# Performance work log

Hardware: AMD Instinct MI355X
Metric: run time of the kernel (lower is better)

## Reference

```python
import jax, jax.numpy as jnp
import numpy as np

VOCAB_SIZE = 32000
HIDDEN_DIM = 1024
NUM_BUF_ACTIONS = 128
BATCH = 64
SEQ_LEN = 512


def setup_inputs() -> dict:
    key = jax.random.key(0)
    ks = jax.random.split(key, 8)
    H = HIDDEN_DIM
    x = jax.random.randint(ks[0], (BATCH, SEQ_LEN), 0, VOCAB_SIZE, dtype=jnp.int32)
    true_actions = jax.random.randint(ks[1], (BATCH, SEQ_LEN), 0, NUM_BUF_ACTIONS, dtype=jnp.int32)
    true_states = jax.random.randint(ks[2], (BATCH, SEQ_LEN), 0, NUM_BUF_ACTIONS, dtype=jnp.int32)
    use_forcing = 0
    # Learned params: embedding table, LSTM input/recurrent kernels (gate order i,f,g,o), dense head
    embed = jax.random.normal(ks[3], (VOCAB_SIZE, H), dtype=jnp.float32) * 0.02
    Wi = jax.random.normal(ks[4], (H, 4 * H), dtype=jnp.float32) * (1.0 / np.sqrt(H))
    Wh = jax.random.normal(ks[5], (H, 4 * H), dtype=jnp.float32) * (1.0 / np.sqrt(H))
    bh = jnp.zeros((4 * H,), dtype=jnp.float32)
    Wo = jax.random.normal(ks[6], (H, NUM_BUF_ACTIONS), dtype=jnp.float32) * (1.0 / np.sqrt(H))
    bo = jnp.zeros((NUM_BUF_ACTIONS,), dtype=jnp.float32)
    return {"embed": embed, "Wi": Wi, "Wh": Wh, "bh": bh, "Wo": Wo, "bo": bo,
            "x": x, "true_actions": true_actions, "true_states": true_states,
            "use_forcing": use_forcing}


def _lstm_forward(embed, Wi, Wh, bh, Wo, bo, x):
    B, S = x.shape
    H = embed.shape[1]
    x_emb = embed[x]                                    # [B,S,H]
    # Precompute input-side gate projections for all timesteps (one big GEMM)
    gx = jnp.einsum('bsh,hg->sbg', x_emb, Wi)           # [S,B,4H]
    c0 = jnp.zeros((B, H), dtype=x_emb.dtype)
    h0 = jnp.zeros((B, H), dtype=x_emb.dtype)

    def step(carry, gx_t):
        c, h = carry
        gates = gx_t + h @ Wh + bh                      # [B,4H]
        i, f, g, o = jnp.split(gates, 4, axis=-1)
        i = jax.nn.sigmoid(i)
        f = jax.nn.sigmoid(f)
        g = jnp.tanh(g)
        o = jax.nn.sigmoid(o)
        c = f * c + i * g
        h = o * jnp.tanh(c)
        return (c, h), h

    _, hs = jax.lax.scan(step, (c0, h0), gx)            # hs: [S,B,H]
    hs = jnp.transpose(hs, (1, 0, 2))                   # [B,S,H]
    logits_buf = hs @ Wo + bo                           # [B,S,A]
    dummy = jnp.zeros((B, S, 1), dtype=logits_buf.dtype)
    return dummy, logits_buf, dummy


def reference(embed, Wi, Wh, bh, Wo, bo, x, true_actions, true_states, use_forcing):
    # true_actions/true_states/use_forcing are unused in the original forward
    return _lstm_forward(embed, Wi, Wh, bh, Wo, bo, x)
```

## Files before the change

kernel.cpp:

```cpp
#include <hip/hip_runtime.h>
#include <hip/hip_bf16.h>

typedef __attribute__((ext_vector_type(8))) short short8;
typedef __attribute__((ext_vector_type(4))) float float4v;
typedef __attribute__((ext_vector_type(4))) unsigned int uint4v;
typedef unsigned short ushort_t;
typedef unsigned int uint_t;

#define BB 64
#define SS 512
#define HH 1024
#define AA 128
#define NWG 256

#define XSW_BYTES   67108864ULL
#define WSW_BYTES   16777216ULL
#define HALL_BYTES  67239936ULL
#define XSW_OFF     0ULL
#define WSW_OFF     (XSW_OFF + XSW_BYTES)
#define HALL_OFF    (WSW_OFF + WSW_BYTES)
#define FLAGS_OFF   (HALL_OFF + HALL_BYTES)

__device__ __forceinline__ ushort_t f2bf(float f) {
    union { float f; uint_t u; } v; v.f = f;
    uint_t u = v.u;
    return (ushort_t)((u + 0x7fffu + ((u >> 16) & 1u)) >> 16);
}

__device__ __forceinline__ float fast_sigmoid(float x) {
    return __builtin_amdgcn_rcpf(1.0f + __expf(-x));
}
__device__ __forceinline__ float fast_tanh(float x) {
    return 1.0f - 2.0f * __builtin_amdgcn_rcpf(1.0f + __expf(2.0f * x));
}

__global__ void k_init(uint_t* __restrict__ flags, ushort_t* __restrict__ hall,
                       float* __restrict__ out) {
    int i = blockIdx.x * 256 + threadIdx.x;
    if (i < NWG) flags[i] = 0u;
    ((uint_t*)hall)[i] = 0u;
    out[i] = 0.0f;
    out[32768 + (size_t)BB * SS * AA + i] = 0.0f;
}

__global__ void k_prep_x(const float* __restrict__ embed, const int* __restrict__ x,
                         ushort_t* __restrict__ xsw) {
    int t = blockIdx.x * 256 + threadIdx.x;
    int lane = t & 63;
    int rg   = (t >> 6) & 3;
    int kk   = (t >> 8) & 31;
    int s    = t >> 13;
    int b  = rg * 16 + (lane & 15);
    int k0 = kk * 32 + (lane >> 4) * 8;
    int tok = x[b * SS + s];
    const float* src = embed + (size_t)tok * HH + k0;
    float4v v0 = *(const float4v*)src;
    float4v v1 = *(const float4v*)(src + 4);
    uint_t p0 = (uint_t)f2bf(v0[0]) | ((uint_t)f2bf(v0[1]) << 16);
    uint_t p1 = (uint_t)f2bf(v0[2]) | ((uint_t)f2bf(v0[3]) << 16);
    uint_t p2 = (uint_t)f2bf(v1[0]) | ((uint_t)f2bf(v1[1]) << 16);
    uint_t p3 = (uint_t)f2bf(v1[2]) | ((uint_t)f2bf(v1[3]) << 16);
    uint4v pk = {p0, p1, p2, p3};
    ((uint4v*)xsw)[t] = pk;
}

__global__ void k_prep_w(const float* __restrict__ Wi, const float* __restrict__ Wh,
                         ushort_t* __restrict__ wsw) {
    int t = blockIdx.x * 256 + threadIdx.x;
    int u = t & 1023;
    int q = (t >> 10) & 3;
    int k = t >> 12;
    float v = (k < 1024) ? Wi[(size_t)k * 4096 + q * 1024 + u]
                         : Wh[(size_t)(k - 1024) * 4096 + q * 1024 + u];
    int g = u >> 2, du = u & 3;
    int c = du * 4 + q;
    int kk = k >> 5, quad = (k >> 3) & 3, j = k & 7;
    int lane = quad * 16 + c;
    wsw[(((size_t)g * 64 + kk) * 64 + lane) * 8 + j] = f2bf(v);
}

__global__ void __launch_bounds__(256)
k_lstm(const ushort_t* __restrict__ xsw, const ushort_t* __restrict__ wsw,
       ushort_t* hall, const float* __restrict__ bh, uint_t* flags) {
    __shared__ ushort_t wlds[64 * 64 * 8];
    const int g    = blockIdx.x;
    const int tid  = threadIdx.x;
    const int lane = tid & 63;
    const int rg   = tid >> 6;

    {
        const uint4v* src = (const uint4v*)(wsw + (size_t)g * 64 * 64 * 8);
        uint4v* dst = (uint4v*)wlds;
        for (int i = tid; i < 4096; i += 256) dst[i] = src[i];
    }
    __syncthreads();

    const int c_idx = lane & 15;
    const int q  = c_idx & 3;
    const int du = c_idx >> 2;
    const int quad = lane >> 4;
    const int u = g * 4 + du;
    const float bhv = bh[q * 1024 + u];

    const int kk_h = u >> 5;
    const int quad_h = (u & 31) >> 3;
    const int j_h = u & 7;
    uint_t* hall32 = (uint_t*)hall;

    float cst0 = 0.f, cst1 = 0.f, cst2 = 0.f, cst3 = 0.f;
    const short8* xbase = (const short8*)xsw;
    const short8* hbase = (const short8*)hall;
    const short8* wl = (const short8*)wlds + lane;

    for (int s = 0; s < SS; ++s) {
        float4v ac0 = {bhv, bhv, bhv, bhv};
        float4v ac1 = {0.f, 0.f, 0.f, 0.f};
        float4v ac2 = {0.f, 0.f, 0.f, 0.f};
        float4v ac3 = {0.f, 0.f, 0.f, 0.f};

        const short8* xp = xbase + (((size_t)s * 32) * 4 + rg) * 64 + lane;
        #pragma unroll
        for (int kk = 0; kk < 32; kk += 4) {
            short8 a0 = xp[(kk + 0) * 256];
            short8 a1 = xp[(kk + 1) * 256];
            short8 a2 = xp[(kk + 2) * 256];
            short8 a3 = xp[(kk + 3) * 256];
            ac0 = __builtin_amdgcn_mfma_f32_16x16x32_bf16(a0, wl[(kk + 0) * 64], ac0, 0, 0, 0);
            ac1 = __builtin_amdgcn_mfma_f32_16x16x32_bf16(a1, wl[(kk + 1) * 64], ac1, 0, 0, 0);
            ac2 = __builtin_amdgcn_mfma_f32_16x16x32_bf16(a2, wl[(kk + 2) * 64], ac2, 0, 0, 0);
            ac3 = __builtin_amdgcn_mfma_f32_16x16x32_bf16(a3, wl[(kk + 3) * 64], ac3, 0, 0, 0);
        }

        {
            bool ok;
            do {
                uint_t f = __hip_atomic_load(&flags[tid], __ATOMIC_RELAXED,
                                             __HIP_MEMORY_SCOPE_AGENT);
                ok = (f >= (uint_t)s);
            } while (!__syncthreads_and(ok));
            asm volatile("" ::: "memory");
        }

        const short8* hp = hbase + (((size_t)s * 32) * 4 + rg) * 64 + lane;
        #pragma unroll
        for (int kk = 0; kk < 32; kk += 4) {
            short8 a0 = hp[(kk + 0) * 256];
            short8 a1 = hp[(kk + 1) * 256];
            short8 a2 = hp[(kk + 2) * 256];
            short8 a3 = hp[(kk + 3) * 256];
            ac0 = __builtin_amdgcn_mfma_f32_16x16x32_bf16(a0, wl[(32 + kk + 0) * 64], ac0, 0, 0, 0);
            ac1 = __builtin_amdgcn_mfma_f32_16x16x32_bf16(a1, wl[(32 + kk + 1) * 64], ac1, 0, 0, 0);
            ac2 = __builtin_amdgcn_mfma_f32_16x16x32_bf16(a2, wl[(32 + kk + 2) * 64], ac2, 0, 0, 0);
            ac3 = __builtin_amdgcn_mfma_f32_16x16x32_bf16(a3, wl[(32 + kk + 3) * 64], ac3, 0, 0, 0);
        }
        float4v acc = (ac0 + ac1) + (ac2 + ac3);

        float hv[4];
        #pragma unroll
        for (int r = 0; r < 4; ++r) {
            float own = acc[r];
            float a = (q == 2) ? fast_tanh(own) : fast_sigmoid(own);
            float x1 = __shfl_xor(a, 1);
            float x2 = __shfl_xor(a, 2);
            float x3 = __shfl_xor(a, 3);
            float gi, gf, gg, go;
            if      (q == 0) { gi = a;  gf = x1; gg = x2; go = x3; }
            else if (q == 1) { gi = x1; gf = a;  gg = x3; go = x2; }
            else if (q == 2) { gi = x2; gf = x3; gg = a;  go = x1; }
            else             { gi = x3; gf = x2; gg = x1; go = a;  }
            float cv = (r == 0 ? cst0 : r == 1 ? cst1 : r == 2 ? cst2 : cst3);
            cv = gf * cv + gi * gg;
            if (r == 0) cst0 = cv; else if (r == 1) cst1 = cv;
            else if (r == 2) cst2 = cv; else cst3 = cv;
            hv[r] = go * fast_tanh(cv);
        }

        float pv0 = __shfl_xor(hv[0], 4);
        float pv1 = __shfl_xor(hv[1], 4);
        float pv2 = __shfl_xor(hv[2], 4);
        float pv3 = __shfl_xor(hv[3], 4);
        if (q == 0 && (du & 1) == 0) {
            float pv[4] = {pv0, pv1, pv2, pv3};
            size_t base = (((size_t)(s + 1) * 32 + kk_h) * 4 + rg) * 64;
            #pragma unroll
            for (int r = 0; r < 4; ++r) {
                uint_t packed = (uint_t)f2bf(hv[r]) | ((uint_t)f2bf(pv[r]) << 16);
                int lane_h = quad_h * 16 + quad * 4 + r;
                size_t idx = ((base + (size_t)lane_h) * 8 + j_h) >> 1;
                __hip_atomic_store(&hall32[idx], packed, __ATOMIC_RELAXED,
                                   __HIP_MEMORY_SCOPE_AGENT);
            }
        }
        __syncthreads();
        if (tid == 0)
            __hip_atomic_store(&flags[g], (uint_t)(s + 1), __ATOMIC_RELAXED,
                               __HIP_MEMORY_SCOPE_AGENT);
    }
}

__global__ void __launch_bounds__(256)
k_head(const ushort_t* __restrict__ hall, const float* __restrict__ Wo,
       const float* __restrict__ bo, float* __restrict__ out) {
    __shared__ ushort_t wlds[32 * 2 * 64 * 8];
    const int wg = blockIdx.x;
    const int cg = wg & 3, sg = wg >> 2;
    const int tid = threadIdx.x, lane = tid & 63, rg = tid >> 6;
    const int col0 = cg * 32;

    for (int i = tid; i < 32768; i += 256) {
        int k = i >> 5;
        int col = i & 31;
        float v = Wo[(size_t)k * AA + col0 + col];
        int kk = k >> 5, quad = (k >> 3) & 3, j = k & 7;
        int nt = col >> 4, cl = col & 15;
        wlds[(((kk * 2 + nt) * 64) + quad * 16 + cl) * 8 + j] = f2bf(v);
    }
    __syncthreads();

    const int cl = lane & 15, quad = lane >> 4;
    const float bo0 = bo[col0 + cl];
    const float bo1 = bo[col0 + 16 + cl];
    const short8* wl = (const short8*)wlds + lane;

    for (int si = 0; si < 4; ++si) {
        int s = sg * 4 + si;
        float4v a0 = {bo0, bo0, bo0, bo0};
        float4v a1 = {bo1, bo1, bo1, bo1};
        const short8* hp = (const short8*)hall + (((size_t)(s + 1) * 32) * 4 + rg) * 64 + lane;
        #pragma unroll 8
        for (int kk = 0; kk < 32; ++kk) {
            short8 a = hp[kk * 256];
            a0 = __builtin_amdgcn_mfma_f32_16x16x32_bf16(a, wl[(kk * 2 + 0) * 64], a0, 0, 0, 0);
            a1 = __builtin_amdgcn_mfma_f32_16x16x32_bf16(a, wl[(kk * 2 + 1) * 64], a1, 0, 0, 0);
        }
        #pragma unroll
        for (int r = 0; r < 4; ++r) {
            int b = rg * 16 + quad * 4 + r;
            size_t o = 32768 + ((size_t)b * SS + s) * AA;
            out[o + col0 + cl]      = a0[r];
            out[o + col0 + 16 + cl] = a1[r];
        }
    }
}

extern "C" void kernel_launch(void* const* d_in, const int* in_sizes, int n_in,
                              void* d_out, int out_size, void* d_ws, size_t ws_size,
                              hipStream_t stream) {
    const float* embed = (const float*)d_in[0];
    const float* Wi    = (const float*)d_in[1];
    const float* Wh    = (const float*)d_in[2];
    const float* bh    = (const float*)d_in[3];
    const float* Wo    = (const float*)d_in[4];
    const float* bo    = (const float*)d_in[5];
    const int*   x     = (const int*)d_in[6];
    float* out = (float*)d_out;
    unsigned char* ws = (unsigned char*)d_ws;

    ushort_t* xsw  = (ushort_t*)(ws + XSW_OFF);
    ushort_t* wsw  = (ushort_t*)(ws + WSW_OFF);
    ushort_t* hall = (ushort_t*)(ws + HALL_OFF);
    uint_t*   flags = (uint_t*)(ws + FLAGS_OFF);

    k_init  <<<128,   256, 0, stream>>>(flags, hall, out);
    k_prep_x<<<16384, 256, 0, stream>>>(embed, x, xsw);
    k_prep_w<<<32768, 256, 0, stream>>>(Wi, Wh, wsw);
    k_lstm  <<<NWG,   256, 0, stream>>>(xsw, wsw, hall, bh, flags);
    k_head  <<<512,   256, 0, stream>>>(hall, Wo, bo, out);
}
```

Before: 2.795 ms.

## Split LSTM into producer WGs for input projections and consumer WGs for recurrence

```diff
diff --git a/kernel.cpp b/kernel.cpp
--- a/kernel.cpp
+++ b/kernel.cpp
@@ -6,12 +6,14 @@
 typedef __attribute__((ext_vector_type(4))) unsigned int uint4v;
 typedef unsigned short ushort_t;
 typedef unsigned int uint_t;
+typedef unsigned long long ull_t;
 
 #define BB 64
 #define SS 512
 #define HH 1024
 #define AA 128
-#define NWG 256
+#define NCG 128
+#define RSLOTS 8
 
 #define XSW_BYTES   67108864ULL
 #define WSW_BYTES   16777216ULL
@@ -20,13 +22,19 @@
 #define WSW_OFF     (XSW_OFF + XSW_BYTES)
 #define HALL_OFF    (WSW_OFF + WSW_BYTES)
 #define FLAGS_OFF   (HALL_OFF + HALL_BYTES)
+#define RING_OFF    (FLAGS_OFF + 4096ULL)
+#define RING_BYTES  (RSLOTS * 128ULL * 2ULL * 256ULL * 8ULL)
+
+#define MFMA __builtin_amdgcn_mfma_f32_16x16x32_bf16
 
 __device__ __forceinline__ ushort_t f2bf(float f) {
     union { float f; uint_t u; } v; v.f = f;
     uint_t u = v.u;
     return (ushort_t)((u + 0x7fffu + ((u >> 16) & 1u)) >> 16);
 }
-
+__device__ __forceinline__ float bf2f(ushort_t u) {
+    union { uint_t u; float f; } v; v.u = (uint_t)u << 16; return v.f;
+}
 __device__ __forceinline__ float fast_sigmoid(float x) {
     return __builtin_amdgcn_rcpf(1.0f + __expf(-x));
 }
@@ -37,7 +45,7 @@
 __global__ void k_init(uint_t* __restrict__ flags, ushort_t* __restrict__ hall,
                        float* __restrict__ out) {
     int i = blockIdx.x * 256 + threadIdx.x;
-    if (i < NWG) flags[i] = 0u;
+    if (i < 256) flags[i] = 0u;
     ((uint_t*)hall)[i] = 0u;
     out[i] = 0.0f;
     out[32768 + (size_t)BB * SS * AA + i] = 0.0f;
@@ -80,18 +88,21 @@
 }
 
 __global__ void __launch_bounds__(256)
-k_lstm(const ushort_t* __restrict__ xsw, const ushort_t* __restrict__ wsw,
-       ushort_t* hall, const float* __restrict__ bh, uint_t* flags) {
-    __shared__ ushort_t wlds[64 * 64 * 8];
-    const int g    = blockIdx.x;
+k_lstm2(const ushort_t* __restrict__ xsw, const ushort_t* __restrict__ wsw,
+        ushort_t* hall, const float* __restrict__ bh, uint_t* flags, ull_t* ring) {
+    __shared__ ushort_t wlds[2 * 32 * 64 * 8 + 11264];
     const int tid  = threadIdx.x;
     const int lane = tid & 63;
     const int rg   = tid >> 6;
+    const bool producer = (blockIdx.x >= NCG);
+    const int  wg = producer ? (blockIdx.x - NCG) : blockIdx.x;
 
     {
-        const uint4v* src = (const uint4v*)(wsw + (size_t)g * 64 * 64 * 8);
+        const int kkoff = producer ? 0 : 32;
+        const uint4v* s0 = (const uint4v*)(wsw + ((size_t)(2 * wg)     * 64 + kkoff) * 512);
+        const uint4v* s1 = (const uint4v*)(wsw + ((size_t)(2 * wg + 1) * 64 + kkoff) * 512);
         uint4v* dst = (uint4v*)wlds;
-        for (int i = tid; i < 4096; i += 256) dst[i] = src[i];
+        for (int i = tid; i < 2048; i += 256) { dst[i] = s0[i]; dst[2048 + i] = s1[i]; }
     }
     __syncthreads();
 
@@ -99,101 +110,149 @@
     const int q  = c_idx & 3;
     const int du = c_idx >> 2;
     const int quad = lane >> 4;
-    const int u = g * 4 + du;
-    const float bhv = bh[q * 1024 + u];
-
-    const int kk_h = u >> 5;
-    const int quad_h = (u & 31) >> 3;
-    const int j_h = u & 7;
+    const short8* wl = (const short8*)wlds + lane;
+
+    if (producer) {
+        const float bhv0 = bh[q * 1024 + (2 * wg)     * 4 + du];
+        const float bhv1 = bh[q * 1024 + (2 * wg + 1) * 4 + du];
+        const short8* xbase = (const short8*)xsw;
+        for (int s = 0; s < SS; ++s) {
+            float4v a00 = {bhv0, bhv0, bhv0, bhv0};
+            float4v a01 = {0.f, 0.f, 0.f, 0.f};
+            float4v a10 = {bhv1, bhv1, bhv1, bhv1};
+            float4v a11 = {0.f, 0.f, 0.f, 0.f};
+            const short8* xp = xbase + (((size_t)s * 32) * 4 + rg) * 64 + lane;
+            #pragma unroll
+            for (int kk = 0; kk < 32; kk += 2) {
+                short8 f0 = xp[(kk + 0) * 256];
+                short8 f1 = xp[(kk + 1) * 256];
+                a00 = MFMA(f0, wl[(kk + 0) * 64], a00, 0, 0, 0);
+                a10 = MFMA(f0, wl[(32 + kk + 0) * 64], a10, 0, 0, 0);
+                a01 = MFMA(f1, wl[(kk + 1) * 64], a01, 0, 0, 0);
+                a11 = MFMA(f1, wl[(32 + kk + 1) * 64], a11, 0, 0, 0);
+            }
+            float4v g0 = a00 + a01;
+            float4v g1 = a10 + a11;
+            {
+                int need = s - (RSLOTS - 1);
+                if (need > 0) {
+                    while ((int)__hip_atomic_load(&flags[wg], __ATOMIC_RELAXED,
+                                                  __HIP_MEMORY_SCOPE_AGENT) < need)
+                        __builtin_amdgcn_s_sleep(2);
+                }
+            }
+            ull_t* rp = ring + ((size_t)(s & (RSLOTS - 1)) * 128 + wg) * 512 + tid;
+            uint_t d0 = (uint_t)f2bf(g0[0]) | ((uint_t)f2bf(g0[1]) << 16);
+            uint_t d1 = (uint_t)f2bf(g0[2]) | ((uint_t)f2bf(g0[3]) << 16);
+            __hip_atomic_store(&rp[0], (ull_t)d0 | ((ull_t)d1 << 32),
+                               __ATOMIC_RELAXED, __HIP_MEMORY_SCOPE_AGENT);
+            uint_t e0 = (uint_t)f2bf(g1[0]) | ((uint_t)f2bf(g1[1]) << 16);
+            uint_t e1 = (uint_t)f2bf(g1[2]) | ((uint_t)f2bf(g1[3]) << 16);
+            __hip_atomic_store(&rp[256], (ull_t)e0 | ((ull_t)e1 << 32),
+                               __ATOMIC_RELAXED, __HIP_MEMORY_SCOPE_AGENT);
+            __syncthreads();
+            if (tid == 0)
+                __hip_atomic_store(&flags[128 + wg], (uint_t)(s + 1),
+                                   __ATOMIC_RELAXED, __HIP_MEMORY_SCOPE_AGENT);
+        }
+        return;
+    }
+
     uint_t* hall32 = (uint_t*)hall;
-
-    float cst0 = 0.f, cst1 = 0.f, cst2 = 0.f, cst3 = 0.f;
-    const short8* xbase = (const short8*)xsw;
     const short8* hbase = (const short8*)hall;
-    const short8* wl = (const short8*)wlds + lane;
+    float cst[2][4];
+    #pragma unroll
+    for (int t = 0; t < 2; ++t)
+        #pragma unroll
+        for (int r = 0; r < 4; ++r) cst[t][r] = 0.f;
 
     for (int s = 0; s < SS; ++s) {
-        float4v ac0 = {bhv, bhv, bhv, bhv};
-        float4v ac1 = {0.f, 0.f, 0.f, 0.f};
-        float4v ac2 = {0.f, 0.f, 0.f, 0.f};
-        float4v ac3 = {0.f, 0.f, 0.f, 0.f};
-
-        const short8* xp = xbase + (((size_t)s * 32) * 4 + rg) * 64 + lane;
-        #pragma unroll
-        for (int kk = 0; kk < 32; kk += 4) {
-            short8 a0 = xp[(kk + 0) * 256];
-            short8 a1 = xp[(kk + 1) * 256];
-            short8 a2 = xp[(kk + 2) * 256];
-            short8 a3 = xp[(kk + 3) * 256];
-            ac0 = __builtin_amdgcn_mfma_f32_16x16x32_bf16(a0, wl[(kk + 0) * 64], ac0, 0, 0, 0);
-            ac1 = __builtin_amdgcn_mfma_f32_16x16x32_bf16(a1, wl[(kk + 1) * 64], ac1, 0, 0, 0);
-            ac2 = __builtin_amdgcn_mfma_f32_16x16x32_bf16(a2, wl[(kk + 2) * 64], ac2, 0, 0, 0);
-            ac3 = __builtin_amdgcn_mfma_f32_16x16x32_bf16(a3, wl[(kk + 3) * 64], ac3, 0, 0, 0);
-        }
-
         {
+            const uint_t* addr = (tid < 128) ? &flags[tid] : &flags[128 + wg];
+            const uint_t need  = (tid < 128) ? (uint_t)s : (uint_t)(s + 1);
             bool ok;
             do {
-                uint_t f = __hip_atomic_load(&flags[tid], __ATOMIC_RELAXED,
+                uint_t f = __hip_atomic_load(addr, __ATOMIC_RELAXED,
                                              __HIP_MEMORY_SCOPE_AGENT);
-                ok = (f >= (uint_t)s);
+                ok = (f >= need);
             } while (!__syncthreads_and(ok));
             asm volatile("" ::: "memory");
         }
 
+        const ull_t* rp = ring + ((size_t)(s & (RSLOTS - 1)) * 128 + wg) * 512 + tid;
+        ull_t gx0 = __hip_atomic_load(&rp[0],   __ATOMIC_RELAXED, __HIP_MEMORY_SCOPE_AGENT);
+        ull_t gx1 = __hip_atomic_load(&rp[256], __ATOMIC_RELAXED, __HIP_MEMORY_SCOPE_AGENT);
+
+        float4v a00 = {0.f, 0.f, 0.f, 0.f};
+        float4v a01 = {0.f, 0.f, 0.f, 0.f};
+        float4v a10 = {0.f, 0.f, 0.f, 0.f};
+        float4v a11 = {0.f, 0.f, 0.f, 0.f};
         const short8* hp = hbase + (((size_t)s * 32) * 4 + rg) * 64 + lane;
         #pragma unroll
-        for (int kk = 0; kk < 32; kk += 4) {
-            short8 a0 = hp[(kk + 0) * 256];
-            short8 a1 = hp[(kk + 1) * 256];
-            short8 a2 = hp[(kk + 2) * 256];
-            short8 a3 = hp[(kk + 3) * 256];
-            ac0 = __builtin_amdgcn_mfma_f32_16x16x32_bf16(a0, wl[(32 + kk + 0) * 64], ac0, 0, 0, 0);
-            ac1 = __builtin_amdgcn_mfma_f32_16x16x32_bf16(a1, wl[(32 + kk + 1) * 64], ac1, 0, 0, 0);
-            ac2 = __builtin_amdgcn_mfma_f32_16x16x32_bf16(a2, wl[(32 + kk + 2) * 64], ac2, 0, 0, 0);
-            ac3 = __builtin_amdgcn_mfma_f32_16x16x32_bf16(a3, wl[(32 + kk + 3) * 64], ac3, 0, 0, 0);
-        }
-        float4v acc = (ac0 + ac1) + (ac2 + ac3);
-
-        float hv[4];
-        #pragma unroll
-        for (int r = 0; r < 4; ++r) {
-            float own = acc[r];
-            float a = (q == 2) ? fast_tanh(own) : fast_sigmoid(own);
-            float x1 = __shfl_xor(a, 1);
-            float x2 = __shfl_xor(a, 2);
-            float x3 = __shfl_xor(a, 3);
-            float gi, gf, gg, go;
-            if      (q == 0) { gi = a;  gf = x1; gg = x2; go = x3; }
-            else if (q == 1) { gi = x1; gf = a;  gg = x3; go = x2; }
-            else if (q == 2) { gi = x2; gf = x3; gg = a;  go = x1; }
-            else             { gi = x3; gf = x2; gg = x1; go = a;  }
-            float cv = (r == 0 ? cst0 : r == 1 ? cst1 : r == 2 ? cst2 : cst3);
-            cv = gf * cv + gi * gg;
-            if (r == 0) cst0 = cv; else if (r == 1) cst1 = cv;
-            else if (r == 2) cst2 = cv; else cst3 = cv;
-            hv[r] = go * fast_tanh(cv);
-        }
-
-        float pv0 = __shfl_xor(hv[0], 4);
-        float pv1 = __shfl_xor(hv[1], 4);
-        float pv2 = __shfl_xor(hv[2], 4);
-        float pv3 = __shfl_xor(hv[3], 4);
-        if (q == 0 && (du & 1) == 0) {
-            float pv[4] = {pv0, pv1, pv2, pv3};
-            size_t base = (((size_t)(s + 1) * 32 + kk_h) * 4 + rg) * 64;
+        for (int kk = 0; kk < 32; kk += 2) {
+            short8 f0 = hp[(kk + 0) * 256];
+            short8 f1 = hp[(kk + 1) * 256];
+            a00 = MFMA(f0, wl[(kk + 0) * 64], a00, 0, 0, 0);
+            a10 = MFMA(f0, wl[(32 + kk + 0) * 64], a10, 0, 0, 0);
+            a01 = MFMA(f1, wl[(kk + 1) * 64], a01, 0, 0, 0);
+            a11 = MFMA(f1, wl[(32 + kk + 1) * 64], a11, 0, 0, 0);
+        }
+        float4v acc0 = a00 + a01;
+        float4v acc1 = a10 + a11;
+        acc0[0] += bf2f((ushort_t)gx0);
+        acc0[1] += bf2f((ushort_t)(gx0 >> 16));
+        acc0[2] += bf2f((ushort_t)(gx0 >> 32));
+        acc0[3] += bf2f((ushort_t)(gx0 >> 48));
+        acc1[0] += bf2f((ushort_t)gx1);
+        acc1[1] += bf2f((ushort_t)(gx1 >> 16));
+        acc1[2] += bf2f((ushort_t)(gx1 >> 32));
+        acc1[3] += bf2f((ushort_t)(gx1 >> 48));
+
+        float hv[2][4];
+        #pragma unroll
+        for (int t = 0; t < 2; ++t) {
             #pragma unroll
             for (int r = 0; r < 4; ++r) {
-                uint_t packed = (uint_t)f2bf(hv[r]) | ((uint_t)f2bf(pv[r]) << 16);
-                int lane_h = quad_h * 16 + quad * 4 + r;
-                size_t idx = ((base + (size_t)lane_h) * 8 + j_h) >> 1;
-                __hip_atomic_store(&hall32[idx], packed, __ATOMIC_RELAXED,
-                                   __HIP_MEMORY_SCOPE_AGENT);
+                float own = t ? acc1[r] : acc0[r];
+                float a = (q == 2) ? fast_tanh(own) : fast_sigmoid(own);
+                float x1 = __shfl_xor(a, 1);
+                float x2 = __shfl_xor(a, 2);
+                float x3 = __shfl_xor(a, 3);
+                float gi, gf, gg, go;
+                if      (q == 0) { gi = a;  gf = x1; gg = x2; go = x3; }
+                else if (q == 1) { gi = x1; gf = a;  gg = x3; go = x2; }
+                else if (q == 2) { gi = x2; gf = x3; gg = a;  go = x1; }
+                else             { gi = x3; gf = x2; gg = x1; go = a;  }
+                float cv = gf * cst[t][r] + gi * gg;
+                cst[t][r] = cv;
+                hv[t][r] = go * fast_tanh(cv);
+            }
+        }
+
+        #pragma unroll
+        for (int t = 0; t < 2; ++t) {
+            float p0 = __shfl_xor(hv[t][0], 4);
+            float p1 = __shfl_xor(hv[t][1], 4);
+            float p2 = __shfl_xor(hv[t][2], 4);
+            float p3 = __shfl_xor(hv[t][3], 4);
+            if (q == 0 && (du & 1) == 0) {
+                int u = (2 * wg + t) * 4 + du;
+                int kk_h = u >> 5, quad_h = (u & 31) >> 3, j_h = u & 7;
+                size_t base = (((size_t)(s + 1) * 32 + kk_h) * 4 + rg) * 64;
+                float pv[4] = {p0, p1, p2, p3};
+                #pragma unroll
+                for (int r = 0; r < 4; ++r) {
+                    uint_t packed = (uint_t)f2bf(hv[t][r]) | ((uint_t)f2bf(pv[r]) << 16);
+                    int lane_h = quad_h * 16 + quad * 4 + r;
+                    size_t idx = ((base + (size_t)lane_h) * 8 + j_h) >> 1;
+                    __hip_atomic_store(&hall32[idx], packed, __ATOMIC_RELAXED,
+                                       __HIP_MEMORY_SCOPE_AGENT);
+                }
             }
         }
         __syncthreads();
         if (tid == 0)
-            __hip_atomic_store(&flags[g], (uint_t)(s + 1), __ATOMIC_RELAXED,
+            __hip_atomic_store(&flags[wg], (uint_t)(s + 1), __ATOMIC_RELAXED,
                                __HIP_MEMORY_SCOPE_AGENT);
     }
 }
@@ -230,8 +289,8 @@
         #pragma unroll 8
         for (int kk = 0; kk < 32; ++kk) {
             short8 a = hp[kk * 256];
-            a0 = __builtin_amdgcn_mfma_f32_16x16x32_bf16(a, wl[(kk * 2 + 0) * 64], a0, 0, 0, 0);
-            a1 = __builtin_amdgcn_mfma_f32_16x16x32_bf16(a, wl[(kk * 2 + 1) * 64], a1, 0, 0, 0);
+            a0 = MFMA(a, wl[(kk * 2 + 0) * 64], a0, 0, 0, 0);
+            a1 = MFMA(a, wl[(kk * 2 + 1) * 64], a1, 0, 0, 0);
         }
         #pragma unroll
         for (int r = 0; r < 4; ++r) {
@@ -256,14 +315,15 @@
     float* out = (float*)d_out;
     unsigned char* ws = (unsigned char*)d_ws;
 
-    ushort_t* xsw  = (ushort_t*)(ws + XSW_OFF);
-    ushort_t* wsw  = (ushort_t*)(ws + WSW_OFF);
-    ushort_t* hall = (ushort_t*)(ws + HALL_OFF);
+    ushort_t* xsw   = (ushort_t*)(ws + XSW_OFF);
+    ushort_t* wsw   = (ushort_t*)(ws + WSW_OFF);
+    ushort_t* hall  = (ushort_t*)(ws + HALL_OFF);
     uint_t*   flags = (uint_t*)(ws + FLAGS_OFF);
+    ull_t*    ring  = (ull_t*)(ws + RING_OFF);
 
     k_init  <<<128,   256, 0, stream>>>(flags, hall, out);
     k_prep_x<<<16384, 256, 0, stream>>>(embed, x, xsw);
     k_prep_w<<<32768, 256, 0, stream>>>(Wi, Wh, wsw);
-    k_lstm  <<<NWG,   256, 0, stream>>>(xsw, wsw, hall, bh, flags);
+    k_lstm2 <<<256,   256, 0, stream>>>(xsw, wsw, hall, bh, flags, ring);
     k_head  <<<512,   256, 0, stream>>>(hall, Wo, bo, out);
 }
```

New measurement: 5.186 ms. +85.6%, slower.

## Split barrier signal and wait around x-projection work in persistent LSTM

Applied to the files above, without the earlier changes.

```diff
diff --git a/kernel.cpp b/kernel.cpp
--- a/kernel.cpp
+++ b/kernel.cpp
@@ -20,6 +20,8 @@
 #define WSW_OFF     (XSW_OFF + XSW_BYTES)
 #define HALL_OFF    (WSW_OFF + WSW_BYTES)
 #define FLAGS_OFF   (HALL_OFF + HALL_BYTES)
+
+#define MFMA __builtin_amdgcn_mfma_f32_16x16x32_bf16
 
 __device__ __forceinline__ ushort_t f2bf(float f) {
     union { float f; uint_t u; } v; v.f = f;
@@ -82,7 +84,7 @@
 __global__ void __launch_bounds__(256)
 k_lstm(const ushort_t* __restrict__ xsw, const ushort_t* __restrict__ wsw,
        ushort_t* hall, const float* __restrict__ bh, uint_t* flags) {
-    __shared__ ushort_t wlds[64 * 64 * 8];
+    __shared__ ushort_t wlds[64 * 64 * 8 + 10240];
     const int g    = blockIdx.x;
     const int tid  = threadIdx.x;
     const int lane = tid & 63;
@@ -106,11 +108,11 @@
     const int quad_h = (u & 31) >> 3;
     const int j_h = u & 7;
     uint_t* hall32 = (uint_t*)hall;
-
-    float cst0 = 0.f, cst1 = 0.f, cst2 = 0.f, cst3 = 0.f;
     const short8* xbase = (const short8*)xsw;
     const short8* hbase = (const short8*)hall;
     const short8* wl = (const short8*)wlds + lane;
+
+    float cst0 = 0.f, cst1 = 0.f, cst2 = 0.f, cst3 = 0.f;
 
     for (int s = 0; s < SS; ++s) {
         float4v ac0 = {bhv, bhv, bhv, bhv};
@@ -119,25 +121,51 @@
         float4v ac3 = {0.f, 0.f, 0.f, 0.f};
 
         const short8* xp = xbase + (((size_t)s * 32) * 4 + rg) * 64 + lane;
-        #pragma unroll
-        for (int kk = 0; kk < 32; kk += 4) {
+
+        #pragma unroll
+        for (int kk = 0; kk < 16; kk += 4) {
             short8 a0 = xp[(kk + 0) * 256];
             short8 a1 = xp[(kk + 1) * 256];
             short8 a2 = xp[(kk + 2) * 256];
             short8 a3 = xp[(kk + 3) * 256];
-            ac0 = __builtin_amdgcn_mfma_f32_16x16x32_bf16(a0, wl[(kk + 0) * 64], ac0, 0, 0, 0);
-            ac1 = __builtin_amdgcn_mfma_f32_16x16x32_bf16(a1, wl[(kk + 1) * 64], ac1, 0, 0, 0);
-            ac2 = __builtin_amdgcn_mfma_f32_16x16x32_bf16(a2, wl[(kk + 2) * 64], ac2, 0, 0, 0);
-            ac3 = __builtin_amdgcn_mfma_f32_16x16x32_bf16(a3, wl[(kk + 3) * 64], ac3, 0, 0, 0);
+            ac0 = MFMA(a0, wl[(kk + 0) * 64], ac0, 0, 0, 0);
+            ac1 = MFMA(a1, wl[(kk + 1) * 64], ac1, 0, 0, 0);
+            ac2 = MFMA(a2, wl[(kk + 2) * 64], ac2, 0, 0, 0);
+            ac3 = MFMA(a3, wl[(kk + 3) * 64], ac3, 0, 0, 0);
+        }
+
+        __syncthreads();
+        if (tid == 0)
+            __hip_atomic_store(&flags[g], (uint_t)s, __ATOMIC_RELAXED,
+                               __HIP_MEMORY_SCOPE_AGENT);
+
+        uint_t f0 = __hip_atomic_load(&flags[lane],       __ATOMIC_RELAXED, __HIP_MEMORY_SCOPE_AGENT);
+        uint_t f1 = __hip_atomic_load(&flags[64 + lane],  __ATOMIC_RELAXED, __HIP_MEMORY_SCOPE_AGENT);
+        uint_t f2 = __hip_atomic_load(&flags[128 + lane], __ATOMIC_RELAXED, __HIP_MEMORY_SCOPE_AGENT);
+        uint_t f3 = __hip_atomic_load(&flags[192 + lane], __ATOMIC_RELAXED, __HIP_MEMORY_SCOPE_AGENT);
+
+        #pragma unroll
+        for (int kk = 16; kk < 32; kk += 4) {
+            short8 a0 = xp[(kk + 0) * 256];
+            short8 a1 = xp[(kk + 1) * 256];
+            short8 a2 = xp[(kk + 2) * 256];
+            short8 a3 = xp[(kk + 3) * 256];
+            ac0 = MFMA(a0, wl[(kk + 0) * 64], ac0, 0, 0, 0);
+            ac1 = MFMA(a1, wl[(kk + 1) * 64], ac1, 0, 0, 0);
+            ac2 = MFMA(a2, wl[(kk + 2) * 64], ac2, 0, 0, 0);
+            ac3 = MFMA(a3, wl[(kk + 3) * 64], ac3, 0, 0, 0);
         }
 
         {
-            bool ok;
-            do {
-                uint_t f = __hip_atomic_load(&flags[tid], __ATOMIC_RELAXED,
-                                             __HIP_MEMORY_SCOPE_AGENT);
-                ok = (f >= (uint_t)s);
-            } while (!__syncthreads_and(ok));
+            const uint_t sn = (uint_t)s;
+            bool ok = (f0 >= sn) & (f1 >= sn) & (f2 >= sn) & (f3 >= sn);
+            while (!__all(ok)) {
+                f0 = __hip_atomic_load(&flags[lane],       __ATOMIC_RELAXED, __HIP_MEMORY_SCOPE_AGENT);
+                f1 = __hip_atomic_load(&flags[64 + lane],  __ATOMIC_RELAXED, __HIP_MEMORY_SCOPE_AGENT);
+                f2 = __hip_atomic_load(&flags[128 + lane], __ATOMIC_RELAXED, __HIP_MEMORY_SCOPE_AGENT);
+                f3 = __hip_atomic_load(&flags[192 + lane], __ATOMIC_RELAXED, __HIP_MEMORY_SCOPE_AGENT);
+                ok = (f0 >= sn) & (f1 >= sn) & (f2 >= sn) & (f3 >= sn);
+            }
             asm volatile("" ::: "memory");
         }
 
@@ -148,10 +176,10 @@
             short8 a1 = hp[(kk + 1) * 256];
             short8 a2 = hp[(kk + 2) * 256];
             short8 a3 = hp[(kk + 3) * 256];
-            ac0 = __builtin_amdgcn_mfma_f32_16x16x32_bf16(a0, wl[(32 + kk + 0) * 64], ac0, 0, 0, 0);
-            ac1 = __builtin_amdgcn_mfma_f32_16x16x32_bf16(a1, wl[(32 + kk + 1) * 64], ac1, 0, 0, 0);
-            ac2 = __builtin_amdgcn_mfma_f32_16x16x32_bf16(a2, wl[(32 + kk + 2) * 64], ac2, 0, 0, 0);
-            ac3 = __builtin_amdgcn_mfma_f32_16x16x32_bf16(a3, wl[(32 + kk + 3) * 64], ac3, 0, 0, 0);
+            ac0 = MFMA(a0, wl[(32 + kk + 0) * 64], ac0, 0, 0, 0);
+            ac1 = MFMA(a1, wl[(32 + kk + 1) * 64], ac1, 0, 0, 0);
+            ac2 = MFMA(a2, wl[(32 + kk + 2) * 64], ac2, 0, 0, 0);
+            ac3 = MFMA(a3, wl[(32 + kk + 3) * 64], ac3, 0, 0, 0);
         }
         float4v acc = (ac0 + ac1) + (ac2 + ac3);
 
@@ -191,10 +219,6 @@
                                    __HIP_MEMORY_SCOPE_AGENT);
             }
         }
-        __syncthreads();
-        if (tid == 0)
-            __hip_atomic_store(&flags[g], (uint_t)(s + 1), __ATOMIC_RELAXED,
-                               __HIP_MEMORY_SCOPE_AGENT);
     }
 }
 
@@ -230,8 +254,8 @@
         #pragma unroll 8
         for (int kk = 0; kk < 32; ++kk) {
             short8 a = hp[kk * 256];
-            a0 = __builtin_amdgcn_mfma_f32_16x16x32_bf16(a, wl[(kk * 2 + 0) * 64], a0, 0, 0, 0);
-            a1 = __builtin_amdgcn_mfma_f32_16x16x32_bf16(a, wl[(kk * 2 + 1) * 64], a1, 0, 0, 0);
+            a0 = MFMA(a, wl[(kk * 2 + 0) * 64], a0, 0, 0, 0);
+            a1 = MFMA(a, wl[(kk * 2 + 1) * 64], a1, 0, 0, 0);
         }
         #pragma unroll
         for (int r = 0; r < 4; ++r) {
```

Result: slower. 5.105 ms (+82.7%).

## Halve recurrent workgroups by assigning two weight slices per workgroup

Applied to the files above, without the earlier changes.

```diff
diff --git a/kernel.cpp b/kernel.cpp
--- a/kernel.cpp
+++ b/kernel.cpp
@@ -11,7 +11,8 @@
 #define SS 512
 #define HH 1024
 #define AA 128
-#define NWG 256
+#define NSL 256
+#define NWG 128
 
 #define XSW_BYTES   67108864ULL
 #define WSW_BYTES   16777216ULL
@@ -20,6 +21,8 @@
 #define WSW_OFF     (XSW_OFF + XSW_BYTES)
 #define HALL_OFF    (WSW_OFF + WSW_BYTES)
 #define FLAGS_OFF   (HALL_OFF + HALL_BYTES)
+
+#define MFMA __builtin_amdgcn_mfma_f32_16x16x32_bf16
 
 __device__ __forceinline__ ushort_t f2bf(float f) {
     union { float f; uint_t u; } v; v.f = f;
@@ -82,16 +85,16 @@
 __global__ void __launch_bounds__(256)
 k_lstm(const ushort_t* __restrict__ xsw, const ushort_t* __restrict__ wsw,
        ushort_t* hall, const float* __restrict__ bh, uint_t* flags) {
-    __shared__ ushort_t wlds[64 * 64 * 8];
+    __shared__ ushort_t wlds[2 * 64 * 64 * 8];
     const int g    = blockIdx.x;
     const int tid  = threadIdx.x;
     const int lane = tid & 63;
     const int rg   = tid >> 6;
 
     {
-        const uint4v* src = (const uint4v*)(wsw + (size_t)g * 64 * 64 * 8);
+        const uint4v* src = (const uint4v*)(wsw + (size_t)(2 * g) * 64 * 64 * 8);
         uint4v* dst = (uint4v*)wlds;
-        for (int i = tid; i < 4096; i += 256) dst[i] = src[i];
+        for (int i = tid; i < 8192; i += 256) dst[i] = src[i];
     }
     __syncthreads();
 
@@ -99,24 +102,29 @@
     const int q  = c_idx & 3;
     const int du = c_idx >> 2;
     const int quad = lane >> 4;
-    const int u = g * 4 + du;
-    const float bhv = bh[q * 1024 + u];
-
-    const int kk_h = u >> 5;
-    const int quad_h = (u & 31) >> 3;
-    const int j_h = u & 7;
+    const float bhv0 = bh[q * 1024 + (2 * g)     * 4 + du];
+    const float bhv1 = bh[q * 1024 + (2 * g + 1) * 4 + du];
+
     uint_t* hall32 = (uint_t*)hall;
-
-    float cst0 = 0.f, cst1 = 0.f, cst2 = 0.f, cst3 = 0.f;
     const short8* xbase = (const short8*)xsw;
     const short8* hbase = (const short8*)hall;
     const short8* wl = (const short8*)wlds + lane;
 
+    float cst[2][4];
+    #pragma unroll
+    for (int t = 0; t < 2; ++t)
+        #pragma unroll
+        for (int r = 0; r < 4; ++r) cst[t][r] = 0.f;
+
     for (int s = 0; s < SS; ++s) {
-        float4v ac0 = {bhv, bhv, bhv, bhv};
-        float4v ac1 = {0.f, 0.f, 0.f, 0.f};
-        float4v ac2 = {0.f, 0.f, 0.f, 0.f};
-        float4v ac3 = {0.f, 0.f, 0.f, 0.f};
+        float4v t0a0 = {bhv0, bhv0, bhv0, bhv0};
+        float4v t0a1 = {0.f, 0.f, 0.f, 0.f};
+        float4v t0a2 = {0.f, 0.f, 0.f, 0.f};
+        float4v t0a3 = {0.f, 0.f, 0.f, 0.f};
+        float4v t1a0 = {bhv1, bhv1, bhv1, bhv1};
+        float4v t1a1 = {0.f, 0.f, 0.f, 0.f};
+        float4v t1a2 = {0.f, 0.f, 0.f, 0.f};
+        float4v t1a3 = {0.f, 0.f, 0.f, 0.f};
 
         const short8* xp = xbase + (((size_t)s * 32) * 4 + rg) * 64 + lane;
         #pragma unroll
@@ -125,16 +133,20 @@
             short8 a1 = xp[(kk + 1) * 256];
             short8 a2 = xp[(kk + 2) * 256];
             short8 a3 = xp[(kk + 3) * 256];
-            ac0 = __builtin_amdgcn_mfma_f32_16x16x32_bf16(a0, wl[(kk + 0) * 64], ac0, 0, 0, 0);
-            ac1 = __builtin_amdgcn_mfma_f32_16x16x32_bf16(a1, wl[(kk + 1) * 64], ac1, 0, 0, 0);
-            ac2 = __builtin_amdgcn_mfma_f32_16x16x32_bf16(a2, wl[(kk + 2) * 64], ac2, 0, 0, 0);
-            ac3 = __builtin_amdgcn_mfma_f32_16x16x32_bf16(a3, wl[(kk + 3) * 64], ac3, 0, 0, 0);
+            t0a0 = MFMA(a0, wl[(kk + 0) * 64], t0a0, 0, 0, 0);
+            t1a0 = MFMA(a0, wl[4096 + (kk + 0) * 64], t1a0, 0, 0, 0);
+            t0a1 = MFMA(a1, wl[(kk + 1) * 64], t0a1, 0, 0, 0);
+            t1a1 = MFMA(a1, wl[4096 + (kk + 1) * 64], t1a1, 0, 0, 0);
+            t0a2 = MFMA(a2, wl[(kk + 2) * 64], t0a2, 0, 0, 0);
+            t1a2 = MFMA(a2, wl[4096 + (kk + 2) * 64], t1a2, 0, 0, 0);
+            t0a3 = MFMA(a3, wl[(kk + 3) * 64], t0a3, 0, 0, 0);
+            t1a3 = MFMA(a3, wl[4096 + (kk + 3) * 64], t1a3, 0, 0, 0);
         }
 
         {
             bool ok;
             do {
-                uint_t f = __hip_atomic_load(&flags[tid], __ATOMIC_RELAXED,
+                uint_t f = __hip_atomic_load(&flags[tid & (NWG - 1)], __ATOMIC_RELAXED,
                                              __HIP_MEMORY_SCOPE_AGENT);
                 ok = (f >= (uint_t)s);
             } while (!__syncthreads_and(ok));
@@ -148,47 +160,58 @@
             short8 a1 = hp[(kk + 1) * 256];
             short8 a2 = hp[(kk + 2) * 256];
             short8 a3 = hp[(kk + 3) * 256];
-            ac0 = __builtin_amdgcn_mfma_f32_16x16x32_bf16(a0, wl[(32 + kk + 0) * 64], ac0, 0, 0, 0);
-            ac1 = __builtin_amdgcn_mfma_f32_16x16x32_bf16(a1, wl[(32 + kk + 1) * 64], ac1, 0, 0, 0);
-            ac2 = __builtin_amdgcn_mfma_f32_16x16x32_bf16(a2, wl[(32 + kk + 2) * 64], ac2, 0, 0, 0);
-            ac3 = __builtin_amdgcn_mfma_f32_16x16x32_bf16(a3, wl[(32 + kk + 3) * 64], ac3, 0, 0, 0);
-        }
-        float4v acc = (ac0 + ac1) + (ac2 + ac3);
-
-        float hv[4];
-        #pragma unroll
-        for (int r = 0; r < 4; ++r) {
-            float own = acc[r];
-            float a = (q == 2) ? fast_tanh(own) : fast_sigmoid(own);
-            float x1 = __shfl_xor(a, 1);
-            float x2 = __shfl_xor(a, 2);
-            float x3 = __shfl_xor(a, 3);
-            float gi, gf, gg, go;
-            if      (q == 0) { gi = a;  gf = x1; gg = x2; go = x3; }
-            else if (q == 1) { gi = x1; gf = a;  gg = x3; go = x2; }
-            else if (q == 2) { gi = x2; gf = x3; gg = a;  go = x1; }
-            else             { gi = x3; gf = x2; gg = x1; go = a;  }
-            float cv = (r == 0 ? cst0 : r == 1 ? cst1 : r == 2 ? cst2 : cst3);
-            cv = gf * cv + gi * gg;
-            if (r == 0) cst0 = cv; else if (r == 1) cst1 = cv;
-            else if (r == 2) cst2 = cv; else cst3 = cv;
-            hv[r] = go * fast_tanh(cv);
-        }
-
-        float pv0 = __shfl_xor(hv[0], 4);
-        float pv1 = __shfl_xor(hv[1], 4);
-        float pv2 = __shfl_xor(hv[2], 4);
-        float pv3 = __shfl_xor(hv[3], 4);
-        if (q == 0 && (du & 1) == 0) {
-            float pv[4] = {pv0, pv1, pv2, pv3};
-            size_t base = (((size_t)(s + 1) * 32 + kk_h) * 4 + rg) * 64;
+            t0a0 = MFMA(a0, wl[(32 + kk + 0) * 64], t0a0, 0, 0, 0);
+            t1a0 = MFMA(a0, wl[4096 + (32 + kk + 0) * 64], t1a0, 0, 0, 0);
+            t0a1 = MFMA(a1, wl[(32 + kk + 1) * 64], t0a1, 0, 0, 0);
+            t1a1 = MFMA(a1, wl[4096 + (32 + kk + 1) * 64], t1a1, 0, 0, 0);
+            t0a2 = MFMA(a2, wl[(32 + kk + 2) * 64], t0a2, 0, 0, 0);
+            t1a2 = MFMA(a2, wl[4096 + (32 + kk + 2) * 64], t1a2, 0, 0, 0);
+            t0a3 = MFMA(a3, wl[(32 + kk + 3) * 64], t0a3, 0, 0, 0);
+            t1a3 = MFMA(a3, wl[4096 + (32 + kk + 3) * 64], t1a3, 0, 0, 0);
+        }
+        float4v acc0 = (t0a0 + t0a1) + (t0a2 + t0a3);
+        float4v acc1 = (t1a0 + t1a1) + (t1a2 + t1a3);
+
+        float hv[2][4];
+        #pragma unroll
+        for (int t = 0; t < 2; ++t) {
             #pragma unroll
             for (int r = 0; r < 4; ++r) {
-                uint_t packed = (uint_t)f2bf(hv[r]) | ((uint_t)f2bf(pv[r]) << 16);
-                int lane_h = quad_h * 16 + quad * 4 + r;
-                size_t idx = ((base + (size_t)lane_h) * 8 + j_h) >> 1;
-                __hip_atomic_store(&hall32[idx], packed, __ATOMIC_RELAXED,
-                                   __HIP_MEMORY_SCOPE_AGENT);
+                float own = t ? acc1[r] : acc0[r];
+                float a = (q == 2) ? fast_tanh(own) : fast_sigmoid(own);
+                float x1 = __shfl_xor(a, 1);
+                float x2 = __shfl_xor(a, 2);
+                float x3 = __shfl_xor(a, 3);
+                float gi, gf, gg, go;
+                if      (q == 0) { gi = a;  gf = x1; gg = x2; go = x3; }
+                else if (q == 1) { gi = x1; gf = a;  gg = x3; go = x2; }
+                else if (q == 2) { gi = x2; gf = x3; gg = a;  go = x1; }
+                else             { gi = x3; gf = x2; gg = x1; go = a;  }
+                float cv = gf * cst[t][r] + gi * gg;
+                cst[t][r] = cv;
+                hv[t][r] = go * fast_tanh(cv);
+            }
+        }
+
+        #pragma unroll
+        for (int t = 0; t < 2; ++t) {
+            float p0 = __shfl_xor(hv[t][0], 4);
+            float p1 = __shfl_xor(hv[t][1], 4);
+            float p2 = __shfl_xor(hv[t][2], 4);
+            float p3 = __shfl_xor(hv[t][3], 4);
+            if (q == 0 && (du & 1) == 0) {
+                int u = (2 * g + t) * 4 + du;
+                int kk_h = u >> 5, quad_h = (u & 31) >> 3, j_h = u & 7;
+                size_t base = (((size_t)(s + 1) * 32 + kk_h) * 4 + rg) * 64;
+                float pv[4] = {p0, p1, p2, p3};
+                #pragma unroll
+                for (int r = 0; r < 4; ++r) {
+                    uint_t packed = (uint_t)f2bf(hv[t][r]) | ((uint_t)f2bf(pv[r]) << 16);
+                    int lane_h = quad_h * 16 + quad * 4 + r;
+                    size_t idx = ((base + (size_t)lane_h) * 8 + j_h) >> 1;
+                    __hip_atomic_store(&hall32[idx], packed, __ATOMIC_RELAXED,
+                                       __HIP_MEMORY_SCOPE_AGENT);
+                }
             }
         }
         __syncthreads();
@@ -230,8 +253,8 @@
         #pragma unroll 8
         for (int kk = 0; kk < 32; ++kk) {
             short8 a = hp[kk * 256];
-            a0 = __builtin_amdgcn_mfma_f32_16x16x32_bf16(a, wl[(kk * 2 + 0) * 64], a0, 0, 0, 0);
-            a1 = __builtin_amdgcn_mfma_f32_16x16x32_bf16(a, wl[(kk * 2 + 1) * 64], a1, 0, 0, 0);
+            a0 = MFMA(a, wl[(kk * 2 + 0) * 64], a0, 0, 0, 0);
+            a1 = MFMA(a, wl[(kk * 2 + 1) * 64], a1, 0, 0, 0);
         }
         #pragma unroll
         for (int r = 0; r < 4; ++r) {
```

New measurement: 4.438 ms. 58.8% more time.
